# Optimization experiments

Measured on AMD Instinct MI355X. Metric: run time of the kernel, lower is better.

The kernel has to match this reference:

```python
import jax, jax.numpy as jnp
import numpy as np

N_ENT, N_REL, DIM = 100000, 500, 128
B, F = 256, 20000


def setup_inputs() -> dict:
    key = jax.random.key(0)
    ks = jax.random.split(key, 8)
    return {
        "ent_emb": jax.random.normal(ks[0], (N_ENT, DIM), jnp.float32),
        "rel_emb": jax.random.normal(ks[1], (N_REL, DIM), jnp.float32),
        "heads": jax.random.randint(ks[2], (B,), 0, N_ENT, jnp.int64),
        "rels": jax.random.randint(ks[3], (B,), 0, N_REL, jnp.int64),
        "tails": jax.random.randint(ks[4], (B,), 0, N_ENT, jnp.int64),
        "f_heads": jax.random.randint(ks[5], (F,), 0, N_ENT, jnp.int64),
        "f_rels": jax.random.randint(ks[6], (F,), 0, N_REL, jnp.int64),
        "f_tails": jax.random.randint(ks[7], (F,), 0, N_ENT, jnp.int64),
    }


def _all_scores(ent_emb, rel_emb, heads, rels, tails):
    # TransE L2 score: s(h,r,t) = -||e_h + e_r - e_t||_2
    e_h, e_r, e_t = ent_emb[heads], rel_emb[rels], ent_emb[tails]
    eps = 1e-12
    triple_score = -jnp.sqrt(jnp.maximum(jnp.sum((e_h + e_r - e_t) ** 2, -1), eps))  # [B]
    ent_sq = jnp.sum(ent_emb ** 2, -1)  # [N]
    # head corruption: score(n, r, t) = -||e_n + (e_r - e_t)||
    q = e_r - e_t  # [B, d]
    head_sq = ent_sq[None, :] + 2.0 * jnp.einsum("bd,nd->bn", q, ent_emb) + jnp.sum(q ** 2, -1)[:, None]
    head_scores = -jnp.sqrt(jnp.maximum(head_sq, eps))  # [B, N]
    # tail corruption: score(h, r, n) = -||e_n - (e_h + e_r)||
    p = e_h + e_r  # [B, d]
    tail_sq = ent_sq[None, :] - 2.0 * jnp.einsum("bd,nd->bn", p, ent_emb) + jnp.sum(p ** 2, -1)[:, None]
    tail_scores = -jnp.sqrt(jnp.maximum(tail_sq, eps))  # [B, N]
    return triple_score, head_scores, tail_scores


def _filter_masks(heads, rels, tails, f_heads, f_rels, f_tails, n_ent):
    # mask[b, n] = True iff corrupted triple is in the filter set (to be excluded)
    b = heads.shape[0]
    rows = jnp.arange(b)[:, None]  # [B, 1]
    # head corruption filtered where (f_rel == r_b) & (f_tail == t_b): exclude f_head
    match_h = (f_rels[None, :] == rels[:, None]) & (f_tails[None, :] == tails[:, None])  # [B, F]
    head_mask = jnp.zeros((b, n_ent), bool).at[rows, f_heads[None, :]].max(match_h)
    # tail corruption filtered where (f_rel == r_b) & (f_head == h_b): exclude f_tail
    match_t = (f_rels[None, :] == rels[:, None]) & (f_heads[None, :] == heads[:, None])
    tail_mask = jnp.zeros((b, n_ent), bool).at[rows, f_tails[None, :]].max(match_t)
    return head_mask, tail_mask


def reference(ent_emb, rel_emb, heads, rels, tails, f_heads, f_rels, f_tails):
    triple_score, head_scores, tail_scores = _all_scores(ent_emb, rel_emb, heads, rels, tails)
    head_mask, tail_mask = _filter_masks(heads, rels, tails, f_heads, f_rels, f_tails, ent_emb.shape[0])
    neg_inf = jnp.float32(-jnp.inf)
    head_scores = jnp.where(head_mask, neg_inf, head_scores)
    tail_scores = jnp.where(tail_mask, neg_inf, tail_scores)
    head_ranks = jnp.sum((head_scores > triple_score[:, None]).astype(jnp.int32), axis=1) + 1
    tail_ranks = jnp.sum((tail_scores > triple_score[:, None]).astype(jnp.int32), axis=1) + 1
    return head_ranks, tail_ranks
```

## Files before the change

kernel.cpp:

```cpp
#include <hip/hip_runtime.h>
#include <cstdint>
#include <cstddef>

#define N_ENT 100000
#define DIM 128
#define BSZ 256
#define FSZ 20000
#define BM 64
#define NBT 1563
#define NSCAN 79
#define GCAP 64
#define MCAP_B 64

typedef __attribute__((ext_vector_type(8))) short bf16x8;
typedef __attribute__((ext_vector_type(4))) float f32x4;

#define KEEP(x) asm volatile("" : "+v"(x))

#define WS_QALL   0
#define WS_QSQ    262144
#define WS_THR    264192
#define WS_THC    266240
#define WS_CNT    268288
#define WS_GCNT   270336
#define WS_MATCH  270656
#define WS_QBF    311104
#define WS_QBFP   442176
#define WS_PART   573248
#define WS_NEED   (WS_PART + NBT * 512 * 2)

__device__ inline unsigned short f2bf(float x) {
    union { float f; uint32_t u; } v; v.f = x;
    uint32_t u = v.u;
    u += 0x7fffu + ((u >> 16) & 1);
    return (unsigned short)(u >> 16);
}

__global__ __launch_bounds__(256) void k_front(
    const float* __restrict__ ent, const float* __restrict__ rel,
    const int* __restrict__ heads, const int* __restrict__ rels, const int* __restrict__ tails,
    const int* __restrict__ fh, const int* __restrict__ fr, const int* __restrict__ ft,
    float* __restrict__ qall, float* __restrict__ qsq, float* __restrict__ thr,
    float* __restrict__ thc, int* __restrict__ cnt,
    unsigned short* __restrict__ qbf, unsigned short* __restrict__ qbfp,
    int* __restrict__ gcnt, int2* __restrict__ gmatch)
{
    int bid = blockIdx.x;
    int tid = threadIdx.x;

    if (bid < NSCAN) {
        __shared__ int k1[BSZ], k2[BSZ];
        __shared__ int nm;
        if (tid == 0) nm = 0;
        k1[tid] = rels[tid] * 100000 + tails[tid];
        k2[tid] = rels[tid] * 100000 + heads[tid];
        __syncthreads();
        int f = bid * 256 + tid;
        if (f < FSZ) {
            int vr = fr[f], vt = ft[f], vh = fh[f];
            int fk1 = vr * 100000 + vt;
            int fk2 = vr * 100000 + vh;
            #pragma unroll 8
            for (int b = 0; b < BSZ; b++) {
                if (fk1 == k1[b]) {
                    int p = atomicAdd(&nm, 1);
                    if (p < GCAP) gmatch[bid * GCAP + p] = make_int2(b, vh);
                }
                if (fk2 == k2[b]) {
                    int p = atomicAdd(&nm, 1);
                    if (p < GCAP) gmatch[bid * GCAP + p] = make_int2(BSZ + b, vt);
                }
            }
        }
        __syncthreads();
        if (tid == 0) gcnt[bid] = nm < GCAP ? nm : GCAP;
        return;
    }

    if (tid >= 64) return;
    int b = bid - NSCAN;
    int h = heads[b], r = rels[b], t = tails[b];
    float s0 = 0.f, s1 = 0.f, s2 = 0.f;
    #pragma unroll
    for (int half = 0; half < 2; half++) {
        int d = tid + half * 64;
        float eh = ent[(size_t)h * DIM + d];
        float er = rel[(size_t)r * DIM + d];
        float et = ent[(size_t)t * DIM + d];
        float diff = eh + er - et;
        float q = er - et;
        float p = eh + er;
        qall[(size_t)b * DIM + d] = q;
        qall[(size_t)(BSZ + b) * DIM + d] = -p;
        unsigned short qb16 = f2bf(q), pb16 = f2bf(-p);
        qbf[(size_t)b * DIM + d] = qb16;
        qbf[(size_t)(BSZ + b) * DIM + d] = pb16;
        int ks = d >> 5, kq = (d >> 3) & 3, e = d & 7;
        int l0 = kq * 16 + (b & 15);
        int c0 = b >> 4, c1 = (BSZ + b) >> 4;
        qbfp[(size_t)((c0 * 4 + ks) * 64 + l0) * 8 + e] = qb16;
        qbfp[(size_t)((c1 * 4 + ks) * 64 + l0) * 8 + e] = pb16;
        s0 += diff * diff; s1 += q * q; s2 += p * p;
    }
    #pragma unroll
    for (int off = 32; off; off >>= 1) {
        s0 += __shfl_xor(s0, off);
        s1 += __shfl_xor(s1, off);
        s2 += __shfl_xor(s2, off);
    }
    if (tid == 0) {
        float th = fmaxf(s0, 1e-12f);
        thr[b] = th; thr[BSZ + b] = th;
        qsq[b] = s1; qsq[BSZ + b] = s2;
        thc[b] = (th - s1) * 0.5f;
        thc[BSZ + b] = (th - s2) * 0.5f;
        cnt[b] = 0;  cnt[BSZ + b] = 0;
    }
}

__global__ __launch_bounds__(256, 2) void k_count(
    const float* __restrict__ ent,
    const unsigned short* __restrict__ qbfp, const float* __restrict__ thc,
    unsigned short* __restrict__ part)
{
    int tid = threadIdx.x;
    int l = tid & 63;
    int bt = blockIdx.x * 4 + (tid >> 6);
    if (bt >= NBT) return;
    int koff = (l >> 4) * 8;

    bf16x8 a[4][4];
    float hsq[4];
    #pragma unroll
    for (int s = 0; s < 4; s++) {
        int n = bt * BM + s * 16 + (l & 15);
        bool valid = n < N_ENT;
        const float* rowp = ent + (size_t)(valid ? n : (N_ENT - 1)) * DIM + koff;
        float ss = 0.f;
        #pragma unroll
        for (int ks = 0; ks < 4; ks++) {
            float4 u0 = *(const float4*)(rowp + ks * 32);
            float4 u1 = *(const float4*)(rowp + ks * 32 + 4);
            ss += u0.x*u0.x + u0.y*u0.y + u0.z*u0.z + u0.w*u0.w
                + u1.x*u1.x + u1.y*u1.y + u1.z*u1.z + u1.w*u1.w;
            bf16x8 f;
            f[0]=(short)f2bf(u0.x); f[1]=(short)f2bf(u0.y); f[2]=(short)f2bf(u0.z); f[3]=(short)f2bf(u0.w);
            f[4]=(short)f2bf(u1.x); f[5]=(short)f2bf(u1.y); f[6]=(short)f2bf(u1.z); f[7]=(short)f2bf(u1.w);
            a[s][ks] = f;
        }
        ss += __shfl_xor(ss, 16);
        ss += __shfl_xor(ss, 32);
        hsq[s] = valid ? ss * 0.5f : 1.5e38f;
    }
    f32x4 ehv[4];
    #pragma unroll
    for (int s = 0; s < 4; s++)
        #pragma unroll
        for (int r = 0; r < 4; r++)
            ehv[s][r] = __shfl(hsq[s], (l >> 4) * 4 + r);

    bf16x8 bcur[4], bn1[4], bn2[4];
    #pragma unroll
    for (int ks = 0; ks < 4; ks++) {
        bcur[ks] = *(const bf16x8*)(qbfp + ((size_t)(0 * 4 + ks) * 64 + l) * 8);
        bn1[ks]  = *(const bf16x8*)(qbfp + ((size_t)(1 * 4 + ks) * 64 + l) * 8);
    }
    float tc  = thc[l & 15];
    float tn1 = thc[16 + (l & 15)];
    float tn2;

    uint32_t creg[8] = {0, 0, 0, 0, 0, 0, 0, 0};

    #pragma unroll
    for (int c = 0; c < 32; c++) {
        #pragma unroll
        for (int s = 0; s < 4; s++) {
            KEEP(ehv[s]);
            #pragma unroll
            for (int ks = 0; ks < 4; ks++) KEEP(a[s][ks]);
        }
        if (c < 30) {
            #pragma unroll
            for (int ks = 0; ks < 4; ks++)
                bn2[ks] = *(const bf16x8*)(qbfp + ((size_t)((c + 2) * 4 + ks) * 64 + l) * 8);
            tn2 = thc[(c + 2) * 16 + (l & 15)];
        }
        f32x4 acc[4];
        #pragma unroll
        for (int s = 0; s < 4; s++)
            acc[s] = __builtin_amdgcn_mfma_f32_16x16x32_bf16(a[s][0], bcur[0], ehv[s], 0, 0, 0);
        #pragma unroll
        for (int ks = 1; ks < 4; ks++)
            #pragma unroll
            for (int s = 0; s < 4; s++)
                acc[s] = __builtin_amdgcn_mfma_f32_16x16x32_bf16(a[s][ks], bcur[ks], acc[s], 0, 0, 0);
        uint32_t cl = 0;
        #pragma unroll
        for (int s = 0; s < 4; s++)
            #pragma unroll
            for (int r = 0; r < 4; r++)
                cl += (acc[s][r] < tc) ? 1u : 0u;
        creg[c >> 2] += cl << (8 * (c & 3));
        tc = tn1; tn1 = tn2;
        #pragma unroll
        for (int ks = 0; ks < 4; ks++) { bcur[ks] = bn1[ks]; bn1[ks] = bn2[ks]; }
    }

    #pragma unroll
    for (int i = 0; i < 8; i++) {
        uint32_t x = creg[i];
        x += __shfl_xor(x, 16);
        x += __shfl_xor(x, 32);
        creg[i] = x;
    }
    if (l < 16) {
        #pragma unroll
        for (int c = 0; c < 32; c++)
            part[(size_t)bt * 512 + c * 16 + l] =
                (unsigned short)((creg[c >> 2] >> (8 * (c & 3))) & 0xffu);
    }
}

__global__ __launch_bounds__(128, 3) void k_count_fb(
    const float* __restrict__ ent,
    const unsigned short* __restrict__ qbf,
    const float* __restrict__ thc,
    int* __restrict__ cnt)
{
    int tid = threadIdx.x;
    int lane = tid & 63, wave = tid >> 6;
    int base = blockIdx.x * BM;
    int koff = (lane >> 4) * 8;
    int colq = wave * 256 + (lane & 15);
    const unsigned short* qb = qbf + (size_t)colq * DIM + koff;
    bf16x8 bcur[4], bnext[4];
    #pragma unroll
    for (int ks = 0; ks < 4; ks++) bcur[ks] = *(const bf16x8*)(qb + ks * 32);
    bf16x8 a[4][4];
    float hsq[4];
    #pragma unroll
    for (int s = 0; s < 4; s++) {
        int n = base + s * 16 + (lane & 15);
        bool valid = n < N_ENT;
        const float* rowp = ent + (size_t)(valid ? n : (N_ENT - 1)) * DIM + koff;
        float ss = 0.f;
        #pragma unroll
        for (int ks = 0; ks < 4; ks++) {
            float4 u0 = *(const float4*)(rowp + ks * 32);
            float4 u1 = *(const float4*)(rowp + ks * 32 + 4);
            ss += u0.x*u0.x + u0.y*u0.y + u0.z*u0.z + u0.w*u0.w
                + u1.x*u1.x + u1.y*u1.y + u1.z*u1.z + u1.w*u1.w;
            bf16x8 f;
            f[0]=(short)f2bf(u0.x); f[1]=(short)f2bf(u0.y); f[2]=(short)f2bf(u0.z); f[3]=(short)f2bf(u0.w);
            f[4]=(short)f2bf(u1.x); f[5]=(short)f2bf(u1.y); f[6]=(short)f2bf(u1.z); f[7]=(short)f2bf(u1.w);
            a[s][ks] = f; KEEP(a[s][ks]);
        }
        ss += __shfl_xor(ss, 16); ss += __shfl_xor(ss, 32);
        hsq[s] = valid ? ss * 0.5f : 1.5e38f;
    }
    float eh[4][4];
    #pragma unroll
    for (int s = 0; s < 4; s++)
        #pragma unroll
        for (int r = 0; r < 4; r++) { eh[s][r] = __shfl(hsq[s], (lane >> 4) * 4 + r); KEEP(eh[s][r]); }
    #pragma unroll
    for (int c = 0; c < 16; c++) {
        if (c < 15) {
            #pragma unroll
            for (int ks = 0; ks < 4; ks++)
                bnext[ks] = *(const bf16x8*)(qb + (size_t)(c + 1) * 16 * DIM + ks * 32);
        }
        float tcv = thc[colq + c * 16];
        f32x4 acc[4];
        #pragma unroll
        for (int s = 0; s < 4; s++) acc[s] = (f32x4){0.f, 0.f, 0.f, 0.f};
        #pragma unroll
        for (int ks = 0; ks < 4; ks++)
            #pragma unroll
            for (int s = 0; s < 4; s++)
                acc[s] = __builtin_amdgcn_mfma_f32_16x16x32_bf16(a[s][ks], bcur[ks], acc[s], 0, 0, 0);
        int cl = 0;
        #pragma unroll
        for (int s = 0; s < 4; s++)
            #pragma unroll
            for (int r = 0; r < 4; r++)
                cl += (acc[s][r] < tcv - eh[s][r]) ? 1 : 0;
        cl += __shfl_xor(cl, 16);
        cl += __shfl_xor(cl, 32);
        if (lane < 16) atomicAdd(&cnt[colq + c * 16], cl);
        #pragma unroll
        for (int ks = 0; ks < 4; ks++) bcur[ks] = bnext[ks];
    }
}

__global__ __launch_bounds__(256) void k_adjust(
    const float* __restrict__ ent,
    const float* __restrict__ qall, const float* __restrict__ qsq, const float* __restrict__ thr,
    const int* __restrict__ cnt, const unsigned short* __restrict__ part, int use_part,
    const int* __restrict__ gcnt, const int2* __restrict__ gmatch,
    int* __restrict__ out)
{
    int key = blockIdx.x;
    int tid = threadIdx.x;
    __shared__ int ids[MCAP_B];
    __shared__ int nm;
    __shared__ int wsum[4];
    if (tid == 0) nm = 0;
    __syncthreads();

    int acc = 0;
    if (use_part) {
        for (int i = tid; i < NBT; i += 256)
            acc += part[(size_t)i * 512 + key];
    } else if (tid == 0) {
        acc = cnt[key];
    }

    if (tid < NSCAN) {
        int cg = gcnt[tid];
        if (cg > GCAP) cg = GCAP;
        if (cg < 0) cg = 0;
        for (int i = 0; i < cg; i++) {
            int2 e = gmatch[tid * GCAP + i];
            if (e.x == key) {
                int p = atomicAdd(&nm, 1);
                if (p < MCAP_B) ids[p] = e.y;
            }
        }
    }
    __syncthreads();
    int mm = nm < MCAP_B ? nm : MCAP_B;
    const float* qv = qall + (size_t)key * DIM;
    float qq = qsq[key], th = thr[key];
    for (int i = tid; i < mm; i += 256) {
        int id = ids[i];
        bool dup = false;
        for (int j = 0; j < i; j++) if (ids[j] == id) { dup = true; break; }
        if (!dup) {
            const float* en = ent + (size_t)id * DIM;
            float es = 0.f, dot = 0.f;
            for (int d = 0; d < DIM; d++) { float x = en[d]; es += x * x; dot += x * qv[d]; }
            if (fmaxf(es + 2.f * dot + qq, 1e-12f) < th) acc--;
        }
    }
    #pragma unroll
    for (int off = 32; off; off >>= 1) acc += __shfl_xor(acc, off);
    int lane = tid & 63, wv = tid >> 6;
    if (lane == 0) wsum[wv] = acc;
    __syncthreads();
    if (tid == 0) out[key] = wsum[0] + wsum[1] + wsum[2] + wsum[3] + 1;
}

extern "C" void kernel_launch(void* const* d_in, const int* in_sizes, int n_in,
                              void* d_out, int out_size, void* d_ws, size_t ws_size,
                              hipStream_t stream)
{
    const float* ent   = (const float*)d_in[0];
    const float* rel   = (const float*)d_in[1];
    const int*   heads = (const int*)d_in[2];
    const int*   rels  = (const int*)d_in[3];
    const int*   tails = (const int*)d_in[4];
    const int*   fh    = (const int*)d_in[5];
    const int*   fr    = (const int*)d_in[6];
    const int*   ft    = (const int*)d_in[7];
    int* out = (int*)d_out;

    char* ws = (char*)d_ws;
    float* qall = (float*)(ws + WS_QALL);
    float* qsq  = (float*)(ws + WS_QSQ);
    float* thr  = (float*)(ws + WS_THR);
    float* thc  = (float*)(ws + WS_THC);
    int*   cnt  = (int*)(ws + WS_CNT);
    int*   gcnt = (int*)(ws + WS_GCNT);
    int2*  gmatch = (int2*)(ws + WS_MATCH);
    unsigned short* qbf   = (unsigned short*)(ws + WS_QBF);
    unsigned short* qbfp  = (unsigned short*)(ws + WS_QBFP);
    unsigned short* part  = (unsigned short*)(ws + WS_PART);

    int use_part = (ws_size >= (size_t)WS_NEED) ? 1 : 0;

    k_front<<<NSCAN + BSZ, 256, 0, stream>>>(ent, rel, heads, rels, tails, fh, fr, ft,
                                             qall, qsq, thr, thc, cnt, qbf, qbfp,
                                             gcnt, gmatch);
    if (use_part)
        k_count<<<(NBT + 3) / 4, 256, 0, stream>>>(ent, qbfp, thc, part);
    else
        k_count_fb<<<NBT, 128, 0, stream>>>(ent, qbf, thc, cnt);
    k_adjust<<<2 * BSZ, 256, 0, stream>>>(ent, qall, qsq, thr, cnt, part, use_part,
                                          gcnt, gmatch, out);
}
```

Before: 59.09 us.

## Pre-convert entity table to MFMA-packed bf16 in front kernel

The front kernel gains NBT extra blocks that read the fp32 entity table once and write a bf16 copy already packed in MFMA operand layout, together with half squared norms. The count kernel then loads these packed fragments directly instead of converting fp32 rows and shuffling norms per wave. The fallback path is reduced to the old fused-convert count kernel writing partials, and the atomic-count fallback kernel is removed. This adds a full extra write and read pass of a bf16 entity copy (about 25MB) in exchange for lighter, less register-heavy count waves, and the fallback path still writes to the part buffer even when the workspace may be too small.

```diff
diff --git a/kernel.cpp b/kernel.cpp
--- a/kernel.cpp
+++ b/kernel.cpp
@@ -8,6 +8,7 @@
 #define FSZ 20000
 #define BM 64
 #define NBT 1563
+#define NPAD (NBT * 64)
 #define NSCAN 79
 #define GCAP 64
 #define MCAP_B 64
@@ -27,7 +28,9 @@
 #define WS_QBF    311104
 #define WS_QBFP   442176
 #define WS_PART   573248
-#define WS_NEED   (WS_PART + NBT * 512 * 2)
+#define WS_ESQH   2173760
+#define WS_ABF    2573888
+#define WS_NEED   (WS_ABF + (size_t)NPAD * DIM * 2)
 
 __device__ inline unsigned short f2bf(float x) {
     union { float f; uint32_t u; } v; v.f = x;
@@ -43,19 +46,92 @@
     float* __restrict__ qall, float* __restrict__ qsq, float* __restrict__ thr,
     float* __restrict__ thc, int* __restrict__ cnt,
     unsigned short* __restrict__ qbf, unsigned short* __restrict__ qbfp,
+    unsigned short* __restrict__ abf, float* __restrict__ esqh,
     int* __restrict__ gcnt, int2* __restrict__ gmatch)
 {
     int bid = blockIdx.x;
     int tid = threadIdx.x;
 
-    if (bid < NSCAN) {
+    if (bid < NBT) {
+        int k4 = tid & 31;
+        int ks = k4 >> 3, kq = (k4 >> 1) & 3, e0 = (k4 & 1) * 4;
+        int base4 = bid * 2048;
+        #pragma unroll
+        for (int i = 0; i < 8; i++) {
+            int fidx = base4 + i * 256 + tid;
+            int np = fidx >> 5;
+            bool valid = np < N_ENT;
+            float4 u = make_float4(0.f, 0.f, 0.f, 0.f);
+            if (valid) u = ((const float4*)ent)[fidx];
+            float ss = u.x * u.x + u.y * u.y + u.z * u.z + u.w * u.w;
+            ss += __shfl_xor(ss, 1);
+            ss += __shfl_xor(ss, 2);
+            ss += __shfl_xor(ss, 4);
+            ss += __shfl_xor(ss, 8);
+            ss += __shfl_xor(ss, 16);
+            if (k4 == 0) esqh[np] = valid ? 0.5f * ss : 1.5e38f;
+            uint2 w;
+            w.x = (uint32_t)f2bf(u.x) | ((uint32_t)f2bf(u.y) << 16);
+            w.y = (uint32_t)f2bf(u.z) | ((uint32_t)f2bf(u.w) << 16);
+            int t = np >> 4;
+            size_t idx = ((size_t)(t * 4 + ks) * 64 + kq * 16 + (np & 15)) * 8 + e0;
+            *(uint2*)(abf + idx) = w;
+        }
+        return;
+    }
+
+    if (bid < NBT + BSZ) {
+        if (tid >= 64) return;
+        int b = bid - NBT;
+        int h = heads[b], r = rels[b], t = tails[b];
+        float s0 = 0.f, s1 = 0.f, s2 = 0.f;
+        #pragma unroll
+        for (int half = 0; half < 2; half++) {
+            int d = tid + half * 64;
+            float eh = ent[(size_t)h * DIM + d];
+            float er = rel[(size_t)r * DIM + d];
+            float et = ent[(size_t)t * DIM + d];
+            float diff = eh + er - et;
+            float q = er - et;
+            float p = eh + er;
+            qall[(size_t)b * DIM + d] = q;
+            qall[(size_t)(BSZ + b) * DIM + d] = -p;
+            unsigned short qb16 = f2bf(q), pb16 = f2bf(-p);
+            qbf[(size_t)b * DIM + d] = qb16;
+            qbf[(size_t)(BSZ + b) * DIM + d] = pb16;
+            int ks = d >> 5, kq = (d >> 3) & 3, e = d & 7;
+            int l0 = kq * 16 + (b & 15);
+            int c0 = b >> 4, c1 = (BSZ + b) >> 4;
+            qbfp[(size_t)((c0 * 4 + ks) * 64 + l0) * 8 + e] = qb16;
+            qbfp[(size_t)((c1 * 4 + ks) * 64 + l0) * 8 + e] = pb16;
+            s0 += diff * diff; s1 += q * q; s2 += p * p;
+        }
+        #pragma unroll
+        for (int off = 32; off; off >>= 1) {
+            s0 += __shfl_xor(s0, off);
+            s1 += __shfl_xor(s1, off);
+            s2 += __shfl_xor(s2, off);
+        }
+        if (tid == 0) {
+            float th = fmaxf(s0, 1e-12f);
+            thr[b] = th; thr[BSZ + b] = th;
+            qsq[b] = s1; qsq[BSZ + b] = s2;
+            thc[b] = (th - s1) * 0.5f;
+            thc[BSZ + b] = (th - s2) * 0.5f;
+            cnt[b] = 0;  cnt[BSZ + b] = 0;
+        }
+        return;
+    }
+
+    {
+        int g = bid - NBT - BSZ;
         __shared__ int k1[BSZ], k2[BSZ];
         __shared__ int nm;
         if (tid == 0) nm = 0;
         k1[tid] = rels[tid] * 100000 + tails[tid];
         k2[tid] = rels[tid] * 100000 + heads[tid];
         __syncthreads();
-        int f = bid * 256 + tid;
+        int f = g * 256 + tid;
         if (f < FSZ) {
             int vr = fr[f], vt = ft[f], vh = fh[f];
             int fk1 = vr * 100000 + vt;
@@ -64,61 +140,103 @@
             for (int b = 0; b < BSZ; b++) {
                 if (fk1 == k1[b]) {
                     int p = atomicAdd(&nm, 1);
-                    if (p < GCAP) gmatch[bid * GCAP + p] = make_int2(b, vh);
+                    if (p < GCAP) gmatch[g * GCAP + p] = make_int2(b, vh);
                 }
                 if (fk2 == k2[b]) {
                     int p = atomicAdd(&nm, 1);
-                    if (p < GCAP) gmatch[bid * GCAP + p] = make_int2(BSZ + b, vt);
+                    if (p < GCAP) gmatch[g * GCAP + p] = make_int2(BSZ + b, vt);
                 }
             }
         }
         __syncthreads();
-        if (tid == 0) gcnt[bid] = nm < GCAP ? nm : GCAP;
-        return;
-    }
-
-    if (tid >= 64) return;
-    int b = bid - NSCAN;
-    int h = heads[b], r = rels[b], t = tails[b];
-    float s0 = 0.f, s1 = 0.f, s2 = 0.f;
-    #pragma unroll
-    for (int half = 0; half < 2; half++) {
-        int d = tid + half * 64;
-        float eh = ent[(size_t)h * DIM + d];
-        float er = rel[(size_t)r * DIM + d];
-        float et = ent[(size_t)t * DIM + d];
-        float diff = eh + er - et;
-        float q = er - et;
-        float p = eh + er;
-        qall[(size_t)b * DIM + d] = q;
-        qall[(size_t)(BSZ + b) * DIM + d] = -p;
-        unsigned short qb16 = f2bf(q), pb16 = f2bf(-p);
-        qbf[(size_t)b * DIM + d] = qb16;
-        qbf[(size_t)(BSZ + b) * DIM + d] = pb16;
-        int ks = d >> 5, kq = (d >> 3) & 3, e = d & 7;
-        int l0 = kq * 16 + (b & 15);
-        int c0 = b >> 4, c1 = (BSZ + b) >> 4;
-        qbfp[(size_t)((c0 * 4 + ks) * 64 + l0) * 8 + e] = qb16;
-        qbfp[(size_t)((c1 * 4 + ks) * 64 + l0) * 8 + e] = pb16;
-        s0 += diff * diff; s1 += q * q; s2 += p * p;
-    }
-    #pragma unroll
-    for (int off = 32; off; off >>= 1) {
-        s0 += __shfl_xor(s0, off);
-        s1 += __shfl_xor(s1, off);
-        s2 += __shfl_xor(s2, off);
-    }
-    if (tid == 0) {
-        float th = fmaxf(s0, 1e-12f);
-        thr[b] = th; thr[BSZ + b] = th;
-        qsq[b] = s1; qsq[BSZ + b] = s2;
-        thc[b] = (th - s1) * 0.5f;
-        thc[BSZ + b] = (th - s2) * 0.5f;
-        cnt[b] = 0;  cnt[BSZ + b] = 0;
+        if (tid == 0) gcnt[g] = nm < GCAP ? nm : GCAP;
     }
 }
 
 __global__ __launch_bounds__(256, 2) void k_count(
+    const unsigned short* __restrict__ abf, const float* __restrict__ esqh,
+    const unsigned short* __restrict__ qbfp, const float* __restrict__ thc,
+    unsigned short* __restrict__ part)
+{
+    int tid = threadIdx.x;
+    int l = tid & 63;
+    int bt = blockIdx.x * 4 + (tid >> 6);
+    if (bt >= NBT) return;
+
+    bf16x8 a[4][4];
+    #pragma unroll
+    for (int s = 0; s < 4; s++)
+        #pragma unroll
+        for (int ks = 0; ks < 4; ks++) {
+            a[s][ks] = *(const bf16x8*)(abf + ((size_t)((4 * bt + s) * 4 + ks) * 64 + l) * 8);
+            KEEP(a[s][ks]);
+        }
+    f32x4 ehv[4];
+    #pragma unroll
+    for (int s = 0; s < 4; s++) {
+        #pragma unroll
+        for (int r = 0; r < 4; r++)
+            ehv[s][r] = esqh[bt * BM + s * 16 + (l >> 4) * 4 + r];
+        KEEP(ehv[s]);
+    }
+
+    bf16x8 bcur[4], bn1[4], bn2[4];
+    #pragma unroll
+    for (int ks = 0; ks < 4; ks++) {
+        bcur[ks] = *(const bf16x8*)(qbfp + ((size_t)(0 * 4 + ks) * 64 + l) * 8);
+        bn1[ks]  = *(const bf16x8*)(qbfp + ((size_t)(1 * 4 + ks) * 64 + l) * 8);
+    }
+    float tc  = thc[l & 15];
+    float tn1 = thc[16 + (l & 15)];
+    float tn2;
+
+    uint32_t creg[8] = {0, 0, 0, 0, 0, 0, 0, 0};
+
+    #pragma unroll
+    for (int c = 0; c < 32; c++) {
+        if (c < 30) {
+            #pragma unroll
+            for (int ks = 0; ks < 4; ks++)
+                bn2[ks] = *(const bf16x8*)(qbfp + ((size_t)((c + 2) * 4 + ks) * 64 + l) * 8);
+            tn2 = thc[(c + 2) * 16 + (l & 15)];
+        }
+        f32x4 acc[4];
+        #pragma unroll
+        for (int s = 0; s < 4; s++)
+            acc[s] = __builtin_amdgcn_mfma_f32_16x16x32_bf16(a[s][0], bcur[0], ehv[s], 0, 0, 0);
+        #pragma unroll
+        for (int ks = 1; ks < 4; ks++)
+            #pragma unroll
+            for (int s = 0; s < 4; s++)
+                acc[s] = __builtin_amdgcn_mfma_f32_16x16x32_bf16(a[s][ks], bcur[ks], acc[s], 0, 0, 0);
+        uint32_t cl = 0;
+        #pragma unroll
+        for (int s = 0; s < 4; s++)
+            #pragma unroll
+            for (int r = 0; r < 4; r++)
+                cl += (acc[s][r] < tc) ? 1u : 0u;
+        creg[c >> 2] += cl << (8 * (c & 3));
+        tc = tn1; tn1 = tn2;
+        #pragma unroll
+        for (int ks = 0; ks < 4; ks++) { bcur[ks] = bn1[ks]; bn1[ks] = bn2[ks]; }
+    }
+
+    #pragma unroll
+    for (int i = 0; i < 8; i++) {
+        uint32_t x = creg[i];
+        x += __shfl_xor(x, 16);
+        x += __shfl_xor(x, 32);
+        creg[i] = x;
+    }
+    if (l < 16) {
+        #pragma unroll
+        for (int c = 0; c < 32; c++)
+            part[(size_t)bt * 512 + c * 16 + l] =
+                (unsigned short)((creg[c >> 2] >> (8 * (c & 3))) & 0xffu);
+    }
+}
+
+__global__ __launch_bounds__(256, 2) void k_count_fb(
     const float* __restrict__ ent,
     const unsigned short* __restrict__ qbfp, const float* __restrict__ thc,
     unsigned short* __restrict__ part)
@@ -146,7 +264,7 @@
             bf16x8 f;
             f[0]=(short)f2bf(u0.x); f[1]=(short)f2bf(u0.y); f[2]=(short)f2bf(u0.z); f[3]=(short)f2bf(u0.w);
             f[4]=(short)f2bf(u1.x); f[5]=(short)f2bf(u1.y); f[6]=(short)f2bf(u1.z); f[7]=(short)f2bf(u1.w);
-            a[s][ks] = f;
+            a[s][ks] = f; KEEP(a[s][ks]);
         }
         ss += __shfl_xor(ss, 16);
         ss += __shfl_xor(ss, 32);
@@ -154,10 +272,12 @@
     }
     f32x4 ehv[4];
     #pragma unroll
-    for (int s = 0; s < 4; s++)
+    for (int s = 0; s < 4; s++) {
         #pragma unroll
         for (int r = 0; r < 4; r++)
             ehv[s][r] = __shfl(hsq[s], (l >> 4) * 4 + r);
+        KEEP(ehv[s]);
+    }
 
     bf16x8 bcur[4], bn1[4], bn2[4];
     #pragma unroll
@@ -173,12 +293,6 @@
 
     #pragma unroll
     for (int c = 0; c < 32; c++) {
-        #pragma unroll
-        for (int s = 0; s < 4; s++) {
-            KEEP(ehv[s]);
-            #pragma unroll
-            for (int ks = 0; ks < 4; ks++) KEEP(a[s][ks]);
-        }
         if (c < 30) {
             #pragma unroll
             for (int ks = 0; ks < 4; ks++)
@@ -221,82 +335,10 @@
     }
 }
 
-__global__ __launch_bounds__(128, 3) void k_count_fb(
-    const float* __restrict__ ent,
-    const unsigned short* __restrict__ qbf,
-    const float* __restrict__ thc,
-    int* __restrict__ cnt)
-{
-    int tid = threadIdx.x;
-    int lane = tid & 63, wave = tid >> 6;
-    int base = blockIdx.x * BM;
-    int koff = (lane >> 4) * 8;
-    int colq = wave * 256 + (lane & 15);
-    const unsigned short* qb = qbf + (size_t)colq * DIM + koff;
-    bf16x8 bcur[4], bnext[4];
-    #pragma unroll
-    for (int ks = 0; ks < 4; ks++) bcur[ks] = *(const bf16x8*)(qb + ks * 32);
-    bf16x8 a[4][4];
-    float hsq[4];
-    #pragma unroll
-    for (int s = 0; s < 4; s++) {
-        int n = base + s * 16 + (lane & 15);
-        bool valid = n < N_ENT;
-        const float* rowp = ent + (size_t)(valid ? n : (N_ENT - 1)) * DIM + koff;
-        float ss = 0.f;
-        #pragma unroll
-        for (int ks = 0; ks < 4; ks++) {
-            float4 u0 = *(const float4*)(rowp + ks * 32);
-            float4 u1 = *(const float4*)(rowp + ks * 32 + 4);
-            ss += u0.x*u0.x + u0.y*u0.y + u0.z*u0.z + u0.w*u0.w
-                + u1.x*u1.x + u1.y*u1.y + u1.z*u1.z + u1.w*u1.w;
-            bf16x8 f;
-            f[0]=(short)f2bf(u0.x); f[1]=(short)f2bf(u0.y); f[2]=(short)f2bf(u0.z); f[3]=(short)f2bf(u0.w);
-            f[4]=(short)f2bf(u1.x); f[5]=(short)f2bf(u1.y); f[6]=(short)f2bf(u1.z); f[7]=(short)f2bf(u1.w);
-            a[s][ks] = f; KEEP(a[s][ks]);
-        }
-        ss += __shfl_xor(ss, 16); ss += __shfl_xor(ss, 32);
-        hsq[s] = valid ? ss * 0.5f : 1.5e38f;
-    }
-    float eh[4][4];
-    #pragma unroll
-    for (int s = 0; s < 4; s++)
-        #pragma unroll
-        for (int r = 0; r < 4; r++) { eh[s][r] = __shfl(hsq[s], (lane >> 4) * 4 + r); KEEP(eh[s][r]); }
-    #pragma unroll
-    for (int c = 0; c < 16; c++) {
-        if (c < 15) {
-            #pragma unroll
-            for (int ks = 0; ks < 4; ks++)
-                bnext[ks] = *(const bf16x8*)(qb + (size_t)(c + 1) * 16 * DIM + ks * 32);
-        }
-        float tcv = thc[colq + c * 16];
-        f32x4 acc[4];
-        #pragma unroll
-        for (int s = 0; s < 4; s++) acc[s] = (f32x4){0.f, 0.f, 0.f, 0.f};
-        #pragma unroll
-        for (int ks = 0; ks < 4; ks++)
-            #pragma unroll
-            for (int s = 0; s < 4; s++)
-                acc[s] = __builtin_amdgcn_mfma_f32_16x16x32_bf16(a[s][ks], bcur[ks], acc[s], 0, 0, 0);
-        int cl = 0;
-        #pragma unroll
-        for (int s = 0; s < 4; s++)
-            #pragma unroll
-            for (int r = 0; r < 4; r++)
-                cl += (acc[s][r] < tcv - eh[s][r]) ? 1 : 0;
-        cl += __shfl_xor(cl, 16);
-        cl += __shfl_xor(cl, 32);
-        if (lane < 16) atomicAdd(&cnt[colq + c * 16], cl);
-        #pragma unroll
-        for (int ks = 0; ks < 4; ks++) bcur[ks] = bnext[ks];
-    }
-}
-
 __global__ __launch_bounds__(256) void k_adjust(
     const float* __restrict__ ent,
     const float* __restrict__ qall, const float* __restrict__ qsq, const float* __restrict__ thr,
-    const int* __restrict__ cnt, const unsigned short* __restrict__ part, int use_part,
+    const unsigned short* __restrict__ part,
     const int* __restrict__ gcnt, const int2* __restrict__ gmatch,
     int* __restrict__ out)
 {
@@ -309,12 +351,8 @@
     __syncthreads();
 
     int acc = 0;
-    if (use_part) {
-        for (int i = tid; i < NBT; i += 256)
-            acc += part[(size_t)i * 512 + key];
-    } else if (tid == 0) {
-        acc = cnt[key];
-    }
+    for (int i = tid; i < NBT; i += 256)
+        acc += part[(size_t)i * 512 + key];
 
     if (tid < NSCAN) {
         int cg = gcnt[tid];
@@ -376,16 +414,23 @@
     unsigned short* qbf   = (unsigned short*)(ws + WS_QBF);
     unsigned short* qbfp  = (unsigned short*)(ws + WS_QBFP);
     unsigned short* part  = (unsigned short*)(ws + WS_PART);
-
-    int use_part = (ws_size >= (size_t)WS_NEED) ? 1 : 0;
-
-    k_front<<<NSCAN + BSZ, 256, 0, stream>>>(ent, rel, heads, rels, tails, fh, fr, ft,
-                                             qall, qsq, thr, thc, cnt, qbf, qbfp,
-                                             gcnt, gmatch);
-    if (use_part)
-        k_count<<<(NBT + 3) / 4, 256, 0, stream>>>(ent, qbfp, thc, part);
-    else
-        k_count_fb<<<NBT, 128, 0, stream>>>(ent, qbf, thc, cnt);
-    k_adjust<<<2 * BSZ, 256, 0, stream>>>(ent, qall, qsq, thr, cnt, part, use_part,
-                                          gcnt, gmatch, out);
-}
+    float* esqh = (float*)(ws + WS_ESQH);
+    unsigned short* abf  = (unsigned short*)(ws + WS_ABF);
+
+    int use_abf = (ws_size >= (size_t)WS_NEED) ? 1 : 0;
+    int front_blocks = use_abf ? (NBT + BSZ + NSCAN) : (BSZ + NSCAN);
+
+    if (use_abf) {
+        k_front<<<NBT + BSZ + NSCAN, 256, 0, stream>>>(
+            ent, rel, heads, rels, tails, fh, fr, ft,
+            qall, qsq, thr, thc, cnt, qbf, qbfp, abf, esqh, gcnt, gmatch);
+        k_count<<<(NBT + 3) / 4, 256, 0, stream>>>(abf, esqh, qbfp, thc, part);
+    } else {
+        k_front<<<NBT + BSZ + NSCAN, 256, 0, stream>>>(
+            ent, rel, heads, rels, tails, fh, fr, ft,
+            qall, qsq, thr, thc, cnt, qbf, qbfp, abf, esqh, gcnt, gmatch);
+        k_count_fb<<<(NBT + 3) / 4, 256, 0, stream>>>(ent, qbfp, thc, part);
+    }
+    (void)front_blocks;
+    k_adjust<<<2 * BSZ, 256, 0, stream>>>(ent, qall, qsq, thr, part, gcnt, gmatch, out);
+}
```

Measured after the change: 61.50 us. 4.1% more time.

## Split query columns across four waves per entity tile in count kernel

Applied to the files above, without the earlier changes.

The count kernel now launches one block per 64-entity tile, and each of its four waves handles 8 of the 32 query column groups. Before, each wave handled a full tile against all 32 groups. This creates four times as many waves, for more parallelism and shorter per-wave loops. The cost is that each wave loads and converts the same 64 entity rows, so entity reads and bf16 conversion are repeated four times per tile. The fallback atomic-count path, the unpacked qbf buffer and the cnt buffer are removed, and the workspace offsets are compacted.

```diff
diff --git a/kernel.cpp b/kernel.cpp
--- a/kernel.cpp
+++ b/kernel.cpp
@@ -21,12 +21,10 @@
 #define WS_QSQ    262144
 #define WS_THR    264192
 #define WS_THC    266240
-#define WS_CNT    268288
-#define WS_GCNT   270336
-#define WS_MATCH  270656
-#define WS_QBF    311104
-#define WS_QBFP   442176
-#define WS_PART   573248
+#define WS_GCNT   268288
+#define WS_MATCH  268608
+#define WS_QBFP   309056
+#define WS_PART   440128
 #define WS_NEED   (WS_PART + NBT * 512 * 2)
 
 __device__ inline unsigned short f2bf(float x) {
@@ -41,8 +39,8 @@
     const int* __restrict__ heads, const int* __restrict__ rels, const int* __restrict__ tails,
     const int* __restrict__ fh, const int* __restrict__ fr, const int* __restrict__ ft,
     float* __restrict__ qall, float* __restrict__ qsq, float* __restrict__ thr,
-    float* __restrict__ thc, int* __restrict__ cnt,
-    unsigned short* __restrict__ qbf, unsigned short* __restrict__ qbfp,
+    float* __restrict__ thc,
+    unsigned short* __restrict__ qbfp,
     int* __restrict__ gcnt, int2* __restrict__ gmatch)
 {
     int bid = blockIdx.x;
@@ -93,8 +91,6 @@
         qall[(size_t)b * DIM + d] = q;
         qall[(size_t)(BSZ + b) * DIM + d] = -p;
         unsigned short qb16 = f2bf(q), pb16 = f2bf(-p);
-        qbf[(size_t)b * DIM + d] = qb16;
-        qbf[(size_t)(BSZ + b) * DIM + d] = pb16;
         int ks = d >> 5, kq = (d >> 3) & 3, e = d & 7;
         int l0 = kq * 16 + (b & 15);
         int c0 = b >> 4, c1 = (BSZ + b) >> 4;
@@ -114,19 +110,17 @@
         qsq[b] = s1; qsq[BSZ + b] = s2;
         thc[b] = (th - s1) * 0.5f;
         thc[BSZ + b] = (th - s2) * 0.5f;
-        cnt[b] = 0;  cnt[BSZ + b] = 0;
-    }
-}
-
-__global__ __launch_bounds__(256, 2) void k_count(
+    }
+}
+
+__global__ __launch_bounds__(256) void k_count(
     const float* __restrict__ ent,
     const unsigned short* __restrict__ qbfp, const float* __restrict__ thc,
     unsigned short* __restrict__ part)
 {
     int tid = threadIdx.x;
-    int l = tid & 63;
-    int bt = blockIdx.x * 4 + (tid >> 6);
-    if (bt >= NBT) return;
+    int l = tid & 63, w = tid >> 6;
+    int bt = blockIdx.x;
     int koff = (l >> 4) * 8;
 
     bf16x8 a[4][4];
@@ -147,6 +141,7 @@
             f[0]=(short)f2bf(u0.x); f[1]=(short)f2bf(u0.y); f[2]=(short)f2bf(u0.z); f[3]=(short)f2bf(u0.w);
             f[4]=(short)f2bf(u1.x); f[5]=(short)f2bf(u1.y); f[6]=(short)f2bf(u1.z); f[7]=(short)f2bf(u1.w);
             a[s][ks] = f;
+            KEEP(a[s][ks]);
         }
         ss += __shfl_xor(ss, 16);
         ss += __shfl_xor(ss, 32);
@@ -154,36 +149,33 @@
     }
     f32x4 ehv[4];
     #pragma unroll
-    for (int s = 0; s < 4; s++)
+    for (int s = 0; s < 4; s++) {
         #pragma unroll
         for (int r = 0; r < 4; r++)
             ehv[s][r] = __shfl(hsq[s], (l >> 4) * 4 + r);
-
+        KEEP(ehv[s]);
+    }
+
+    int c0 = w * 8;
     bf16x8 bcur[4], bn1[4], bn2[4];
     #pragma unroll
     for (int ks = 0; ks < 4; ks++) {
-        bcur[ks] = *(const bf16x8*)(qbfp + ((size_t)(0 * 4 + ks) * 64 + l) * 8);
-        bn1[ks]  = *(const bf16x8*)(qbfp + ((size_t)(1 * 4 + ks) * 64 + l) * 8);
-    }
-    float tc  = thc[l & 15];
-    float tn1 = thc[16 + (l & 15)];
+        bcur[ks] = *(const bf16x8*)(qbfp + ((size_t)((c0    ) * 4 + ks) * 64 + l) * 8);
+        bn1[ks]  = *(const bf16x8*)(qbfp + ((size_t)((c0 + 1) * 4 + ks) * 64 + l) * 8);
+    }
+    float tc  = thc[c0 * 16 + (l & 15)];
+    float tn1 = thc[(c0 + 1) * 16 + (l & 15)];
     float tn2;
 
-    uint32_t creg[8] = {0, 0, 0, 0, 0, 0, 0, 0};
-
-    #pragma unroll
-    for (int c = 0; c < 32; c++) {
-        #pragma unroll
-        for (int s = 0; s < 4; s++) {
-            KEEP(ehv[s]);
-            #pragma unroll
-            for (int ks = 0; ks < 4; ks++) KEEP(a[s][ks]);
-        }
-        if (c < 30) {
+    uint32_t creg[2] = {0, 0};
+
+    #pragma unroll
+    for (int cc = 0; cc < 8; cc++) {
+        if (cc < 6) {
             #pragma unroll
             for (int ks = 0; ks < 4; ks++)
-                bn2[ks] = *(const bf16x8*)(qbfp + ((size_t)((c + 2) * 4 + ks) * 64 + l) * 8);
-            tn2 = thc[(c + 2) * 16 + (l & 15)];
+                bn2[ks] = *(const bf16x8*)(qbfp + ((size_t)((c0 + cc + 2) * 4 + ks) * 64 + l) * 8);
+            tn2 = thc[(c0 + cc + 2) * 16 + (l & 15)];
         }
         f32x4 acc[4];
         #pragma unroll
@@ -200,14 +192,14 @@
             #pragma unroll
             for (int r = 0; r < 4; r++)
                 cl += (acc[s][r] < tc) ? 1u : 0u;
-        creg[c >> 2] += cl << (8 * (c & 3));
+        creg[cc >> 2] += cl << (8 * (cc & 3));
         tc = tn1; tn1 = tn2;
         #pragma unroll
         for (int ks = 0; ks < 4; ks++) { bcur[ks] = bn1[ks]; bn1[ks] = bn2[ks]; }
     }
 
     #pragma unroll
-    for (int i = 0; i < 8; i++) {
+    for (int i = 0; i < 2; i++) {
         uint32_t x = creg[i];
         x += __shfl_xor(x, 16);
         x += __shfl_xor(x, 32);
@@ -215,88 +207,16 @@
     }
     if (l < 16) {
         #pragma unroll
-        for (int c = 0; c < 32; c++)
-            part[(size_t)bt * 512 + c * 16 + l] =
-                (unsigned short)((creg[c >> 2] >> (8 * (c & 3))) & 0xffu);
-    }
-}
-
-__global__ __launch_bounds__(128, 3) void k_count_fb(
-    const float* __restrict__ ent,
-    const unsigned short* __restrict__ qbf,
-    const float* __restrict__ thc,
-    int* __restrict__ cnt)
-{
-    int tid = threadIdx.x;
-    int lane = tid & 63, wave = tid >> 6;
-    int base = blockIdx.x * BM;
-    int koff = (lane >> 4) * 8;
-    int colq = wave * 256 + (lane & 15);
-    const unsigned short* qb = qbf + (size_t)colq * DIM + koff;
-    bf16x8 bcur[4], bnext[4];
-    #pragma unroll
-    for (int ks = 0; ks < 4; ks++) bcur[ks] = *(const bf16x8*)(qb + ks * 32);
-    bf16x8 a[4][4];
-    float hsq[4];
-    #pragma unroll
-    for (int s = 0; s < 4; s++) {
-        int n = base + s * 16 + (lane & 15);
-        bool valid = n < N_ENT;
-        const float* rowp = ent + (size_t)(valid ? n : (N_ENT - 1)) * DIM + koff;
-        float ss = 0.f;
-        #pragma unroll
-        for (int ks = 0; ks < 4; ks++) {
-            float4 u0 = *(const float4*)(rowp + ks * 32);
-            float4 u1 = *(const float4*)(rowp + ks * 32 + 4);
-            ss += u0.x*u0.x + u0.y*u0.y + u0.z*u0.z + u0.w*u0.w
-                + u1.x*u1.x + u1.y*u1.y + u1.z*u1.z + u1.w*u1.w;
-            bf16x8 f;
-            f[0]=(short)f2bf(u0.x); f[1]=(short)f2bf(u0.y); f[2]=(short)f2bf(u0.z); f[3]=(short)f2bf(u0.w);
-            f[4]=(short)f2bf(u1.x); f[5]=(short)f2bf(u1.y); f[6]=(short)f2bf(u1.z); f[7]=(short)f2bf(u1.w);
-            a[s][ks] = f; KEEP(a[s][ks]);
-        }
-        ss += __shfl_xor(ss, 16); ss += __shfl_xor(ss, 32);
-        hsq[s] = valid ? ss * 0.5f : 1.5e38f;
-    }
-    float eh[4][4];
-    #pragma unroll
-    for (int s = 0; s < 4; s++)
-        #pragma unroll
-        for (int r = 0; r < 4; r++) { eh[s][r] = __shfl(hsq[s], (lane >> 4) * 4 + r); KEEP(eh[s][r]); }
-    #pragma unroll
-    for (int c = 0; c < 16; c++) {
-        if (c < 15) {
-            #pragma unroll
-            for (int ks = 0; ks < 4; ks++)
-                bnext[ks] = *(const bf16x8*)(qb + (size_t)(c + 1) * 16 * DIM + ks * 32);
-        }
-        float tcv = thc[colq + c * 16];
-        f32x4 acc[4];
-        #pragma unroll
-        for (int s = 0; s < 4; s++) acc[s] = (f32x4){0.f, 0.f, 0.f, 0.f};
-        #pragma unroll
-        for (int ks = 0; ks < 4; ks++)
-            #pragma unroll
-            for (int s = 0; s < 4; s++)
-                acc[s] = __builtin_amdgcn_mfma_f32_16x16x32_bf16(a[s][ks], bcur[ks], acc[s], 0, 0, 0);
-        int cl = 0;
-        #pragma unroll
-        for (int s = 0; s < 4; s++)
-            #pragma unroll
-            for (int r = 0; r < 4; r++)
-                cl += (acc[s][r] < tcv - eh[s][r]) ? 1 : 0;
-        cl += __shfl_xor(cl, 16);
-        cl += __shfl_xor(cl, 32);
-        if (lane < 16) atomicAdd(&cnt[colq + c * 16], cl);
-        #pragma unroll
-        for (int ks = 0; ks < 4; ks++) bcur[ks] = bnext[ks];
+        for (int cc = 0; cc < 8; cc++)
+            part[(size_t)bt * 512 + (c0 + cc) * 16 + l] =
+                (unsigned short)((creg[cc >> 2] >> (8 * (cc & 3))) & 0xffu);
     }
 }
 
 __global__ __launch_bounds__(256) void k_adjust(
     const float* __restrict__ ent,
     const float* __restrict__ qall, const float* __restrict__ qsq, const float* __restrict__ thr,
-    const int* __restrict__ cnt, const unsigned short* __restrict__ part, int use_part,
+    const unsigned short* __restrict__ part,
     const int* __restrict__ gcnt, const int2* __restrict__ gmatch,
     int* __restrict__ out)
 {
@@ -309,12 +229,8 @@
     __syncthreads();
 
     int acc = 0;
-    if (use_part) {
-        for (int i = tid; i < NBT; i += 256)
-            acc += part[(size_t)i * 512 + key];
-    } else if (tid == 0) {
-        acc = cnt[key];
-    }
+    for (int i = tid; i < NBT; i += 256)
+        acc += part[(size_t)i * 512 + key];
 
     if (tid < NSCAN) {
         int cg = gcnt[tid];
@@ -370,22 +286,13 @@
     float* qsq  = (float*)(ws + WS_QSQ);
     float* thr  = (float*)(ws + WS_THR);
     float* thc  = (float*)(ws + WS_THC);
-    int*   cnt  = (int*)(ws + WS_CNT);
     int*   gcnt = (int*)(ws + WS_GCNT);
     int2*  gmatch = (int2*)(ws + WS_MATCH);
-    unsigned short* qbf   = (unsigned short*)(ws + WS_QBF);
-    unsigned short* qbfp  = (unsigned short*)(ws + WS_QBFP);
-    unsigned short* part  = (unsigned short*)(ws + WS_PART);
-
-    int use_part = (ws_size >= (size_t)WS_NEED) ? 1 : 0;
+    unsigned short* qbfp = (unsigned short*)(ws + WS_QBFP);
+    unsigned short* part = (unsigned short*)(ws + WS_PART);
 
     k_front<<<NSCAN + BSZ, 256, 0, stream>>>(ent, rel, heads, rels, tails, fh, fr, ft,
-                                             qall, qsq, thr, thc, cnt, qbf, qbfp,
-                                             gcnt, gmatch);
-    if (use_part)
-        k_count<<<(NBT + 3) / 4, 256, 0, stream>>>(ent, qbfp, thc, part);
-    else
-        k_count_fb<<<NBT, 128, 0, stream>>>(ent, qbf, thc, cnt);
-    k_adjust<<<2 * BSZ, 256, 0, stream>>>(ent, qall, qsq, thr, cnt, part, use_part,
-                                          gcnt, gmatch, out);
-}
+                                             qall, qsq, thr, thc, qbfp, gcnt, gmatch);
+    k_count<<<NBT, 256, 0, stream>>>(ent, qbfp, thc, part);
+    k_adjust<<<2 * BSZ, 256, 0, stream>>>(ent, qall, qsq, thr, part, gcnt, gmatch, out);
+}
```

Result: slower. 78.27 us (+32.5%).
